# Kernel optimization log

Measured on AMD Instinct MI355X. Metric: run time of the kernel, lower is better.

Reference implementation:

```python
import jax, jax.numpy as jnp
import numpy as np

jax.config.update("jax_enable_x64", True)

N_QUBITS = 21
N_LAYERS = 2
N_PARAMS = (N_LAYERS + 1) * N_QUBITS  # 63

# CNOT in |ctrl,tgt> basis, reshaped to (c_out, t_out, c_in, t_in)
_CNOT = jnp.array([[1, 0, 0, 0],
                   [0, 1, 0, 0],
                   [0, 0, 0, 1],
                   [0, 0, 1, 0]], dtype=jnp.complex128).reshape(2, 2, 2, 2)


def _ry(theta):
    # RY(theta) = [[cos(t/2), -sin(t/2)], [sin(t/2), cos(t/2)]]
    c = jnp.cos(theta * 0.5).astype(jnp.complex128)
    s = jnp.sin(theta * 0.5).astype(jnp.complex128)
    return jnp.stack([jnp.stack([c, -s]), jnp.stack([s, c])])


def _apply_1q(state, gate, q):
    # Contract 2x2 gate into qubit axis q of the (2,)*n state tensor.
    state = jnp.tensordot(gate, state, axes=((1,), (q,)))
    return jnp.moveaxis(state, 0, q)


def _apply_cnot(state, q):
    # CNOT with control q, target q+1 (qubit 0 = most-significant axis).
    state = jnp.tensordot(_CNOT, state, axes=((2, 3), (q, q + 1)))
    return jnp.moveaxis(state, (0, 1), (q, q + 1))


def setup_inputs() -> dict:
    key = jax.random.key(0)
    params = jax.random.uniform(key, (N_PARAMS,), dtype=jnp.float32) * (2.0 * np.pi)
    return {"params": params}


def reference(params):
    p = params.astype(jnp.float64)
    # |0...0> as a (2,)*n tensor
    state = jnp.zeros((2,) * N_QUBITS, dtype=jnp.complex128)
    state = state.at[(0,) * N_QUBITS].set(1.0 + 0.0j)
    idx = 0
    for _ in range(N_LAYERS):
        for q in range(N_QUBITS):
            state = _apply_1q(state, _ry(p[idx]), q)
            idx += 1
        for q in range(N_QUBITS - 1):
            state = _apply_cnot(state, q)
    for q in range(N_QUBITS):
        state = _apply_1q(state, _ry(p[idx]), q)
        idx += 1
    state = state.reshape(-1)  # (2**N_QUBITS,)
    return state / jnp.linalg.norm(state)
```

## Files before the change

kernel.cpp:

```cpp
#include <hip/hip_runtime.h>


#define NQ 21
#define NSTATE (1 << NQ)

typedef float f32x2 __attribute__((ext_vector_type(2)));

template <int BIT, int N>
__device__ __forceinline__ void ry_bf(float (&v)[N], float c, float s) {
#pragma unroll
  for (int m = 0; m < N; ++m)
    if ((m & (1 << BIT)) == 0) {
      float a = v[m], b = v[m | (1 << BIT)];
      v[m] = c * a - s * b;
      v[m | (1 << BIT)] = s * a + c * b;
    }
}

template <int CBIT, int TBIT, int N>
__device__ __forceinline__ void cnot_rr(float (&v)[N]) {
#pragma unroll
  for (int m = 0; m < N; ++m)
    if ((m & (1 << CBIT)) && !(m & (1 << TBIT))) {
      float t = v[m];
      v[m] = v[m | (1 << TBIT)];
      v[m | (1 << TBIT)] = t;
    }
}

template <int MASK, int N>
__device__ __forceinline__ void ry_shfl(float (&u)[N], float c, float s,
                                        int lane) {
  const float ss = (lane & MASK) ? s : -s;
#pragma unroll
  for (int e = 0; e < N; ++e) {
    float w = __shfl_xor(u[e], MASK);
    u[e] = c * u[e] + ss * w;
  }
}

template <int CMASK, int TMASK, int N>
__device__ __forceinline__ void cnot_shfl(float (&u)[N], int lane) {
  const bool ctrl = (lane & CMASK) != 0;
#pragma unroll
  for (int e = 0; e < N; ++e) {
    float w = __shfl_xor(u[e], TMASK);
    u[e] = ctrl ? w : u[e];
  }
}

__global__ __launch_bounds__(256, 4) void fused(const float* __restrict__ p,
                                                float* __restrict__ out,
                                                int outmode) {
  __shared__ float2 csn[63];
  const int tid = threadIdx.x;
  if (tid < 63) {
    float h = 0.5f * p[tid];
    csn[tid] = float2{cosf(h), sinf(h)};
  }
  __syncthreads();

  const int lane = tid & 63;
  const int slab = (blockIdx.x << 2) | (tid >> 6);

  float W[2][2];
  {
    const int b0 = (slab >> 11) & 1;
    const float2 g30 = csn[42], g20 = csn[21], g10 = csn[0];
    const float r00 = b0 ? g30.y : g30.x;
    const float r01 = b0 ? g30.x : -g30.y;
    float w00 = r00 * g20.x * g10.x;
    float w01 = r00 * (-g20.y) * g10.y;
    float w10 = r01 * g20.y * g10.x;
    float w11 = r01 * g20.x * g10.y;
#pragma unroll
    for (int q = 1; q <= 11; ++q) {
      const int bq = (slab >> (11 - q)) & 1;
      const float2 g1 = csn[q], g2 = csn[21 + q], g3 = csn[42 + q];
      const float c1 = g1.x, s1 = g1.y;
      const float c2 = g2.x, s2 = g2.y;
      const float c3 = g3.x, s3 = g3.y;
      const float h00 = c1 * w00 + s1 * w01;
      const float h01 = c1 * w10 + s1 * w11;
      const float h10 = s1 * w00 + c1 * w01;
      const float h11 = s1 * w10 + c1 * w11;
      const float m00 = c2 * h00 + s2 * h01;
      const float m01 = s2 * h00 + c2 * h01;
      const float m10 = -s2 * h10 + c2 * h11;
      const float m11 = c2 * h10 - s2 * h11;
      const float r0 = bq ? s3 : c3;
      const float r1 = bq ? c3 : -s3;
      w00 = r0 * m00;
      w01 = r0 * m10;
      w10 = r1 * m01;
      w11 = r1 * m11;
    }
    const float2 g1b = csn[12], g2b = csn[33], gW = csn[13];
    const float hh00 = g1b.x * w00 + g1b.y * w01;
    const float hh01 = g1b.x * w10 + g1b.y * w11;
    const float hh10 = g1b.y * w00 + g1b.x * w01;
    const float hh11 = g1b.y * w10 + g1b.x * w11;
    const float a00 = g2b.x * hh00 + g2b.y * hh01;
    const float a10 = g2b.y * hh00 + g2b.x * hh01;
    const float a01 = -g2b.y * hh10 + g2b.x * hh11;
    const float a11 = g2b.x * hh10 - g2b.y * hh11;
    W[0][0] = a00 * gW.x + a01 * gW.y;
    W[0][1] = a00 * gW.y + a01 * gW.x;
    W[1][0] = a10 * gW.x + a11 * gW.y;
    W[1][1] = a10 * gW.y + a11 * gW.x;
  }

  float v[8];
  {
    const int gl = lane ^ (lane >> 1);
    float tlane = 1.0f;
#pragma unroll
    for (int b = 0; b < 5; ++b) {
      const float2 gb = csn[20 - b];
      tlane *= ((gl >> b) & 1) ? gb.y : gb.x;
    }
    const int x5 = (lane >> 5) & 1;
    const float2 g15 = csn[15], g14 = csn[14];
    const float s15_0 = x5 ? g15.y : g15.x;
    const float s15_1 = x5 ? g15.x : g15.y;
#pragma unroll
    for (int r = 0; r < 8; ++r) {
      float prod = tlane * W[(r >> 2) & 1][(r >> 1) & 1];
      prod *= (r & 1) ? s15_1 : s15_0;
      prod *= ((r ^ (r >> 1)) & 1) ? g14.y : g14.x;
      v[r] = prod;
    }
  }

  ry_bf<1>(v, csn[34].x, csn[34].y);
  ry_bf<0>(v, csn[35].x, csn[35].y);
  ry_shfl<32>(v, csn[36].x, csn[36].y, lane);
  ry_shfl<16>(v, csn[37].x, csn[37].y, lane);
  ry_shfl<8>(v, csn[38].x, csn[38].y, lane);
  ry_shfl<4>(v, csn[39].x, csn[39].y, lane);
  ry_shfl<2>(v, csn[40].x, csn[40].y, lane);
  ry_shfl<1>(v, csn[41].x, csn[41].y, lane);
  cnot_rr<2, 1>(v);
  cnot_rr<1, 0>(v);
  v[1] = __shfl_xor(v[1], 32);
  v[3] = __shfl_xor(v[3], 32);
  v[5] = __shfl_xor(v[5], 32);
  v[7] = __shfl_xor(v[7], 32);
  cnot_shfl<32, 16>(v, lane);
  cnot_shfl<16, 8>(v, lane);
  cnot_shfl<8, 4>(v, lane);
  cnot_shfl<4, 2>(v, lane);
  cnot_shfl<2, 1>(v, lane);
  ry_bf<2>(v, csn[54].x, csn[54].y);
  ry_bf<1>(v, csn[55].x, csn[55].y);
  ry_bf<0>(v, csn[56].x, csn[56].y);
  ry_shfl<32>(v, csn[57].x, csn[57].y, lane);
  ry_shfl<16>(v, csn[58].x, csn[58].y, lane);
  ry_shfl<8>(v, csn[59].x, csn[59].y, lane);
  ry_shfl<4>(v, csn[60].x, csn[60].y, lane);
  ry_shfl<2>(v, csn[61].x, csn[61].y, lane);
  ry_shfl<1>(v, csn[62].x, csn[62].y, lane);

  const int base = (slab << 9) | lane;
  if (outmode == 2) {
    f32x2* o2 = (f32x2*)out;
#pragma unroll
    for (int r = 0; r < 8; ++r) {
      f32x2 w = {v[r], 0.0f};
      __builtin_nontemporal_store(w, &o2[base + (r << 6)]);
    }
  } else {
#pragma unroll
    for (int r = 0; r < 8; ++r)
      __builtin_nontemporal_store(v[r], &out[base + (r << 6)]);
  }
}

extern "C" void kernel_launch(void* const* d_in, const int* in_sizes, int n_in,
                              void* d_out, int out_size, void* d_ws,
                              size_t ws_size, hipStream_t stream) {
  const float* p = (const float*)d_in[0];
  float* out = (float*)d_out;
  const int outmode = (out_size == 2 * NSTATE) ? 2 : 1;
  fused<<<1024, 256, 0, stream>>>(p, out, outmode);
}
```

Baseline: 62.33 us.

## Replace cross-lane shuffles with LDS transposes and vectorize output stores

Stops running the low-qubit RY and CNOT gates through many __shfl_xor ops. Instead the per-wave state is transposed twice through a padded LDS buffer, so most gates act on register-resident bits and only a few shuffles remain. After the second transpose each lane holds 8 contiguous amplitudes, which allows 16-byte vector nontemporal stores. The cost is added LDS traffic and per-wave scratch memory. The transposes rely only on s_waitcnt with no barrier, since each wave uses its own region.

```diff
diff --git a/kernel.cpp b/kernel.cpp
--- a/kernel.cpp
+++ b/kernel.cpp
@@ -3,8 +3,9 @@
 
 #define NQ 21
 #define NSTATE (1 << NQ)
-
-typedef float f32x2 __attribute__((ext_vector_type(2)));
+#define SW(t) ((t) + ((t) >> 5))
+
+typedef float f32x4 __attribute__((ext_vector_type(4)));
 
 template <int BIT, int N>
 __device__ __forceinline__ void ry_bf(float (&v)[N], float c, float s) {
@@ -28,6 +29,17 @@
     }
 }
 
+template <int TBIT, int N>
+__device__ __forceinline__ void cswap_bf(float (&v)[N], bool cond) {
+#pragma unroll
+  for (int m = 0; m < N; ++m)
+    if ((m & (1 << TBIT)) == 0) {
+      float a = v[m], b = v[m | (1 << TBIT)];
+      v[m] = cond ? b : a;
+      v[m | (1 << TBIT)] = cond ? a : b;
+    }
+}
+
 template <int MASK, int N>
 __device__ __forceinline__ void ry_shfl(float (&u)[N], float c, float s,
                                         int lane) {
@@ -39,20 +51,11 @@
   }
 }
 
-template <int CMASK, int TMASK, int N>
-__device__ __forceinline__ void cnot_shfl(float (&u)[N], int lane) {
-  const bool ctrl = (lane & CMASK) != 0;
-#pragma unroll
-  for (int e = 0; e < N; ++e) {
-    float w = __shfl_xor(u[e], TMASK);
-    u[e] = ctrl ? w : u[e];
-  }
-}
-
 __global__ __launch_bounds__(256, 4) void fused(const float* __restrict__ p,
                                                 float* __restrict__ out,
                                                 int outmode) {
   __shared__ float2 csn[63];
+  __shared__ float ex[4][528];
   const int tid = threadIdx.x;
   if (tid < 63) {
     float h = 0.5f * p[tid];
@@ -62,6 +65,7 @@
 
   const int lane = tid & 63;
   const int slab = (blockIdx.x << 2) | (tid >> 6);
+  float* const exw = &ex[tid >> 6][0];
 
   float W[2][2];
   {
@@ -134,45 +138,74 @@
 
   ry_bf<1>(v, csn[34].x, csn[34].y);
   ry_bf<0>(v, csn[35].x, csn[35].y);
-  ry_shfl<32>(v, csn[36].x, csn[36].y, lane);
-  ry_shfl<16>(v, csn[37].x, csn[37].y, lane);
-  ry_shfl<8>(v, csn[38].x, csn[38].y, lane);
-  ry_shfl<4>(v, csn[39].x, csn[39].y, lane);
-  ry_shfl<2>(v, csn[40].x, csn[40].y, lane);
-  ry_shfl<1>(v, csn[41].x, csn[41].y, lane);
   cnot_rr<2, 1>(v);
   cnot_rr<1, 0>(v);
-  v[1] = __shfl_xor(v[1], 32);
-  v[3] = __shfl_xor(v[3], 32);
-  v[5] = __shfl_xor(v[5], 32);
-  v[7] = __shfl_xor(v[7], 32);
-  cnot_shfl<32, 16>(v, lane);
-  cnot_shfl<16, 8>(v, lane);
-  cnot_shfl<8, 4>(v, lane);
-  cnot_shfl<4, 2>(v, lane);
-  cnot_shfl<2, 1>(v, lane);
   ry_bf<2>(v, csn[54].x, csn[54].y);
   ry_bf<1>(v, csn[55].x, csn[55].y);
-  ry_bf<0>(v, csn[56].x, csn[56].y);
-  ry_shfl<32>(v, csn[57].x, csn[57].y, lane);
-  ry_shfl<16>(v, csn[58].x, csn[58].y, lane);
-  ry_shfl<8>(v, csn[59].x, csn[59].y, lane);
-  ry_shfl<4>(v, csn[60].x, csn[60].y, lane);
-  ry_shfl<2>(v, csn[61].x, csn[61].y, lane);
-  ry_shfl<1>(v, csn[62].x, csn[62].y, lane);
-
-  const int base = (slab << 9) | lane;
+
+#pragma unroll
+  for (int r = 0; r < 8; ++r)
+    exw[(r << 6) | (lane ^ (r << 3))] = v[r];
+  asm volatile("s_waitcnt lgkmcnt(0)" ::: "memory");
+  {
+    const int h = lane >> 3, w = lane & 7;
+#pragma unroll
+    for (int r = 0; r < 8; ++r)
+      v[r] = exw[(h << 6) | ((r ^ h) << 3) | w];
+  }
+
+  ry_bf<2>(v, csn[36].x, csn[36].y);
+  ry_bf<1>(v, csn[37].x, csn[37].y);
+  ry_bf<0>(v, csn[38].x, csn[38].y);
+  cswap_bf<2>(v, (lane & 8) != 0);
+  cnot_rr<2, 1>(v);
+  cnot_rr<1, 0>(v);
+  ry_shfl<8>(v, csn[56].x, csn[56].y, lane);
+  ry_bf<2>(v, csn[57].x, csn[57].y);
+  ry_bf<1>(v, csn[58].x, csn[58].y);
+
+  asm volatile("s_waitcnt lgkmcnt(0)" ::: "memory");
+  {
+    const int h = lane >> 3, w = lane & 7;
+#pragma unroll
+    for (int r = 0; r < 8; ++r) {
+      const int t = (h << 6) | (r << 3) | w;
+      exw[SW(t)] = v[r];
+    }
+  }
+  asm volatile("s_waitcnt lgkmcnt(0)" ::: "memory");
+#pragma unroll
+  for (int r = 0; r < 8; ++r) {
+    const int t = (lane << 3) | r;
+    v[r] = exw[SW(t)];
+  }
+
+  ry_bf<2>(v, csn[39].x, csn[39].y);
+  ry_bf<1>(v, csn[40].x, csn[40].y);
+  ry_bf<0>(v, csn[41].x, csn[41].y);
+  cswap_bf<2>(v, (lane & 1) != 0);
+  cnot_rr<2, 1>(v);
+  cnot_rr<1, 0>(v);
+  ry_shfl<1>(v, csn[59].x, csn[59].y, lane);
+  ry_bf<2>(v, csn[60].x, csn[60].y);
+  ry_bf<1>(v, csn[61].x, csn[61].y);
+  ry_bf<0>(v, csn[62].x, csn[62].y);
+
+  const int base = (slab << 9) | (lane << 3);
   if (outmode == 2) {
-    f32x2* o2 = (f32x2*)out;
-#pragma unroll
-    for (int r = 0; r < 8; ++r) {
-      f32x2 w = {v[r], 0.0f};
-      __builtin_nontemporal_store(w, &o2[base + (r << 6)]);
+    f32x4* o4 = (f32x4*)out;
+#pragma unroll
+    for (int i = 0; i < 4; ++i) {
+      f32x4 w = {v[2 * i], 0.0f, v[2 * i + 1], 0.0f};
+      __builtin_nontemporal_store(w, &o4[(base >> 1) + i]);
     }
   } else {
-#pragma unroll
-    for (int r = 0; r < 8; ++r)
-      __builtin_nontemporal_store(v[r], &out[base + (r << 6)]);
+    f32x4* o4 = (f32x4*)(out + base);
+#pragma unroll
+    for (int j = 0; j < 2; ++j) {
+      f32x4 w = {v[4 * j], v[4 * j + 1], v[4 * j + 2], v[4 * j + 3]};
+      __builtin_nontemporal_store(w, &o4[j]);
+    }
   }
 }
 
```

New measurement: 58.97 us. -5.4%, faster.
